# Performance work log

Measured on AMD Instinct MI355X. Metric: run time of the kernel, lower is better.

## Reference

```python
import jax, jax.numpy as jnp
import numpy as np

N_NODES = 20000
N_EDGES = 40000
NODE_DIM = 5
EDGE_DIM = 6
HIDDEN = 64
N_GRAPHS = 500
NODES_PER_GRAPH = 40
TORSIONS = 10
ACTION_DIM = 6


def _lstm_cell(x, h, c, wih, whh, bih, bhh):
    g = x @ wih.T + bih + h @ whh.T + bhh
    i, f, gg, o = jnp.split(g, 4, axis=-1)
    c = jax.nn.sigmoid(f) * c + jax.nn.sigmoid(i) * jnp.tanh(gg)
    return jax.nn.sigmoid(o) * jnp.tanh(c), c


def _gru_cell(x, h, wih, whh, bih, bhh):
    gi = x @ wih.T + bih
    gh = h @ whh.T + bhh
    ir, iz, inn = jnp.split(gi, 3, axis=-1)
    hr, hz, hn = jnp.split(gh, 3, axis=-1)
    r = jax.nn.sigmoid(ir + hr)
    z = jax.nn.sigmoid(iz + hz)
    n = jnp.tanh(inn + r * hn)
    return (1.0 - z) * n + z * h


def setup_inputs() -> dict:
    key = jax.random.key(0)
    ks = jax.random.split(key, 20)
    def gl(k, shape, fan_in):
        return jax.random.normal(k, shape, dtype=jnp.float32) / np.sqrt(float(fan_in))
    H = HIDDEN
    inp = {}
    inp['x'] = jax.random.normal(ks[0], (N_NODES, NODE_DIM), dtype=jnp.float32)
    inp['edge_attr'] = jax.random.normal(ks[1], (N_EDGES, EDGE_DIM), dtype=jnp.float32)
    inp['edge_index'] = jax.random.randint(ks[2], (2, N_EDGES), 0, N_NODES)
    inp['batch'] = jnp.arange(N_NODES) // NODES_PER_GRAPH
    g = jnp.arange(N_GRAPHS * TORSIONS) // TORSIONS
    inp['nrbidx'] = g
    local = jax.random.randint(ks[3], (N_GRAPHS * TORSIONS, 4), 0, NODES_PER_GRAPH)
    inp['nonring'] = local + (g * NODES_PER_GRAPH)[:, None]
    inp['lin0_w'] = gl(ks[4], (H, NODE_DIM), NODE_DIM); inp['lin0_b'] = jnp.zeros(H)
    inp['enn_w1'] = gl(ks[5], (128, EDGE_DIM), EDGE_DIM); inp['enn_b1'] = jnp.zeros(128)
    inp['enn_w2'] = gl(ks[6], (H * H, 128), 128) * 0.1; inp['enn_b2'] = jnp.zeros(H * H)
    inp['conv_root'] = gl(ks[7], (H, H), H); inp['conv_bias'] = jnp.zeros(H)
    inp['gru_wih'] = gl(ks[8], (3 * H, H), H); inp['gru_whh'] = gl(ks[9], (3 * H, H), H)
    inp['gru_bih'] = jnp.zeros(3 * H); inp['gru_bhh'] = jnp.zeros(3 * H)
    inp['s2s_wih'] = gl(ks[10], (4 * H, 2 * H), 2 * H); inp['s2s_whh'] = gl(ks[11], (4 * H, H), H)
    inp['s2s_bih'] = jnp.zeros(4 * H); inp['s2s_bhh'] = jnp.zeros(4 * H)
    inp['mem_wih'] = gl(ks[12], (4 * H, 2 * H), 2 * H); inp['mem_whh'] = gl(ks[13], (4 * H, H), H)
    inp['mem_bih'] = jnp.zeros(4 * H); inp['mem_bhh'] = jnp.zeros(4 * H)
    inp['mlp_w1'] = gl(ks[14], (H, 5 * H), 5 * H); inp['mlp_b1'] = jnp.zeros(H)
    inp['mlp_w2'] = gl(ks[15], (ACTION_DIM, H), H); inp['mlp_b2'] = jnp.zeros(ACTION_DIM)
    return inp


def _forward(x, edge_attr, edge_index, batch, nonring, nrbidx,
             lin0_w, lin0_b, enn_w1, enn_b1, enn_w2, enn_b2, conv_root, conv_bias,
             gru_wih, gru_whh, gru_bih, gru_bhh,
             s2s_wih, s2s_whh, s2s_bih, s2s_bhh,
             mem_wih, mem_whh, mem_bih, mem_bhh,
             mlp_w1, mlp_b1, mlp_w2, mlp_b2):
    n_nodes = x.shape[0]
    H = lin0_w.shape[0]
    N = N_GRAPHS
    src, dst = edge_index[0], edge_index[1]
    out = jax.nn.relu(x @ lin0_w.T + lin0_b)                                   # [n_nodes, H]
    ew = (jax.nn.relu(edge_attr @ enn_w1.T + enn_b1) @ enn_w2.T + enn_b2)
    ew = ew.reshape(-1, H, H)                                                  # [E, H, H] (edge-attr only -> hoisted out of loop)
    deg = jnp.maximum(jax.ops.segment_sum(jnp.ones((edge_index.shape[1],), x.dtype), dst, num_segments=n_nodes), 1.0)
    h = out
    for _ in range(6):
        msg = jnp.einsum('eh,ehk->ek', out[src], ew)                           # per-edge message
        agg = jax.ops.segment_sum(msg, dst, num_segments=n_nodes) / deg[:, None]
        m = jax.nn.relu(agg + out @ conv_root + conv_bias)
        h = _gru_cell(m, h, gru_wih, gru_whh, gru_bih, gru_bhh)
        out = h
    # --- Set2Set pooling, 6 processing steps ---
    q_star = jnp.zeros((N, 2 * H), x.dtype)
    hs = jnp.zeros((N, H), x.dtype)
    cs = jnp.zeros((N, H), x.dtype)
    for _ in range(6):
        hs, cs = _lstm_cell(q_star, hs, cs, s2s_wih, s2s_whh, s2s_bih, s2s_bhh)
        e = jnp.sum(out * hs[batch], axis=-1)                                  # [n_nodes]
        emax = jax.ops.segment_max(e, batch, num_segments=N)
        a = jnp.exp(e - emax[batch])
        a = a / jax.ops.segment_sum(a, batch, num_segments=N)[batch]
        r = jax.ops.segment_sum(a[:, None] * out, batch, num_segments=N)
        q_star = jnp.concatenate([hs, r], axis=-1)                             # [N, 2H]
    # --- memory LSTM (one step, zero initial state) ---
    hx = jnp.zeros((N, H), x.dtype)
    cx = jnp.zeros((N, H), x.dtype)
    hx, cx = _lstm_cell(q_star, hx, cx, mem_wih, mem_whh, mem_bih, mem_bhh)
    # --- gather + concat + MLP + reshape to padded [N, T, A] ---
    t_mem = hx[nrbidx]                                                         # [n_torsions, H]
    t_nodes = out[nonring.reshape(-1)].reshape(-1, 4 * H)                      # [n_torsions, 4H]
    feat = jnp.concatenate([t_mem, t_nodes], axis=-1)                          # [n_torsions, 5H]
    logits = jax.nn.relu(feat @ mlp_w1.T + mlp_b1) @ mlp_w2.T + mlp_b2
    logit = logits.reshape(N, TORSIONS, -1)                                    # uniform torsion_list_sizes -> pad_sequence is a reshape
    return logit, hx[None], cx[None]


def reference(x, edge_attr, edge_index, batch, nonring, nrbidx,
              lin0_w, lin0_b, enn_w1, enn_b1, enn_w2, enn_b2, conv_root, conv_bias,
              gru_wih, gru_whh, gru_bih, gru_bhh,
              s2s_wih, s2s_whh, s2s_bih, s2s_bhh,
              mem_wih, mem_whh, mem_bih, mem_bhh,
              mlp_w1, mlp_b1, mlp_w2, mlp_b2):
    return _forward(x, edge_attr, edge_index, batch, nonring, nrbidx,
                    lin0_w, lin0_b, enn_w1, enn_b1, enn_w2, enn_b2, conv_root, conv_bias,
                    gru_wih, gru_whh, gru_bih, gru_bhh,
                    s2s_wih, s2s_whh, s2s_bih, s2s_bhh,
                    mem_wih, mem_whh, mem_bih, mem_bhh,
                    mlp_w1, mlp_b1, mlp_w2, mlp_b2)
```

## Files before the change

kernel.cpp:

```cpp
#include <hip/hip_runtime.h>
#include <hip/hip_bf16.h>
#include <stdint.h>

#define N_NODES 20000
#define N_EDGES 40000
#define NODE_DIM 5
#define EDGE_DIM 6
#define HID 64
#define N_GRAPHS 500
#define NPG 40
#define TORSIONS 10
#define N_TORS (N_GRAPHS * TORSIONS)
#define ACT 6

typedef short short8 __attribute__((ext_vector_type(8)));
typedef float f32x4 __attribute__((ext_vector_type(4)));

__device__ __forceinline__ float sigmoidf_(float x) { return 1.0f / (1.0f + __expf(-x)); }
__device__ __forceinline__ float dot4(float4 a, float4 b) {
    return a.x * b.x + a.y * b.y + a.z * b.z + a.w * b.w;
}

__global__ void k_lin0(const float* __restrict__ x, const float* __restrict__ w,
                       const float* __restrict__ b, float* __restrict__ out) {
    int i = blockIdx.x * blockDim.x + threadIdx.x;
    int n = i >> 6, k = i & 63;
    const float* xr = x + n * NODE_DIM;
    const float* wr = w + k * NODE_DIM;
    float s = b[k];
#pragma unroll
    for (int d = 0; d < NODE_DIM; ++d) s += xr[d] * wr[d];
    out[i] = fmaxf(s, 0.0f);
}

__global__ void k_h1(const float* __restrict__ ea, const float* __restrict__ w1,
                     const float* __restrict__ b1, __hip_bfloat16* __restrict__ h1b) {
    int i = blockIdx.x * blockDim.x + threadIdx.x;
    int e = i >> 7, j = i & 127;
    const float* er = ea + e * EDGE_DIM;
    const float* wr = w1 + j * EDGE_DIM;
    float s = b1[j];
#pragma unroll
    for (int d = 0; d < EDGE_DIM; ++d) s += er[d] * wr[d];
    h1b[i] = __float2bfloat16(fmaxf(s, 0.0f));
}

__global__ void k_prep(const float* __restrict__ w2, const float* __restrict__ b2,
                       __hip_bfloat16* __restrict__ w2pb, __hip_bfloat16* __restrict__ b2pb) {
    int i = blockIdx.x * blockDim.x + threadIdx.x;
    int cp = i >> 7, j = i & 127;
    int c = ((cp & 63) << 6) | (cp >> 6);
    w2pb[i] = __float2bfloat16(w2[c * 128 + j]);
    if (j == 0) b2pb[cp] = __float2bfloat16(b2[c]);
}

__global__ void k_prep2(const float* __restrict__ cr, const float* __restrict__ wih,
                        const float* __restrict__ whh,
                        __hip_bfloat16* __restrict__ crTb, __hip_bfloat16* __restrict__ wihb,
                        __hip_bfloat16* __restrict__ whhb) {
    int i = blockIdx.x * blockDim.x + threadIdx.x;
    if (i < 12288) {
        wihb[i] = __float2bfloat16(wih[i]);
    } else if (i < 24576) {
        whhb[i - 12288] = __float2bfloat16(whh[i - 12288]);
    } else if (i < 24576 + 4096) {
        int t = i - 24576;
        int c = t >> 6, h = t & 63;
        crTb[t] = __float2bfloat16(cr[h * 64 + c]);
    }
}

__global__ void k_deg(const int* __restrict__ ei, int* __restrict__ degi) {
    int e = blockIdx.x * blockDim.x + threadIdx.x;
    if (e >= N_EDGES) return;
    atomicAdd(&degi[ei[N_EDGES + e]], 1);
}

#define SCAN_C 79
__global__ __launch_bounds__(256) void k_scan(const int* __restrict__ degi,
                                              int* __restrict__ rowptr, int* __restrict__ cursor) {
    __shared__ int part[256];
    int t = threadIdx.x;
    int base = t * SCAN_C;
    int s = 0;
    for (int i = 0; i < SCAN_C; ++i) {
        int idx = base + i;
        if (idx < N_NODES) s += degi[idx];
    }
    part[t] = s;
    __syncthreads();
    for (int off = 1; off < 256; off <<= 1) {
        int v = (t >= off) ? part[t - off] : 0;
        __syncthreads();
        part[t] += v;
        __syncthreads();
    }
    int run = part[t] - s;
    for (int i = 0; i < SCAN_C; ++i) {
        int idx = base + i;
        if (idx < N_NODES) {
            rowptr[idx] = run;
            cursor[idx] = run;
            run += degi[idx];
        }
    }
    if (t == 0) rowptr[N_NODES] = N_EDGES;
}

__global__ void k_fill(const int* __restrict__ ei, int* __restrict__ cursor,
                       int* __restrict__ csr) {
    int e = blockIdx.x * blockDim.x + threadIdx.x;
    if (e >= N_EDGES) return;
    int d = ei[N_EDGES + e];
    int pos = atomicAdd(&cursor[d], 1);
    csr[pos] = e;
}

#define EPB 5
__global__ __launch_bounds__(512) void k_edge_msg(
    const int* __restrict__ ei, const float* __restrict__ out,
    const __hip_bfloat16* __restrict__ h1b, const __hip_bfloat16* __restrict__ w2pb,
    const __hip_bfloat16* __restrict__ b2pb, float* __restrict__ msg) {
    __shared__ __align__(16) short aS[64 * 17 * 8];
    __shared__ __align__(16) float oS[64 * 68];
    __shared__ __align__(16) float mS[64 * 9];
    int bid = blockIdx.x;
    int xg = bid & 7, kb = (bid >> 3) & 7, eg = bid >> 6;
    int ebg = eg * 8 + xg;
    if (ebg >= 125) return;
    int tid = threadIdx.x, w = tid >> 6, lane = tid & 63;
    int lm = lane & 15, lk = lane >> 4;
    int kt = (kb << 3) + w;
    const short8* W8 = (const short8*)w2pb;
    short8 afr[4][4];
#pragma unroll
    for (int hi = 0; hi < 4; ++hi)
#pragma unroll
        for (int ks = 0; ks < 4; ++ks)
            afr[hi][ks] = W8[(size_t)(kt * 64 + hi * 16 + lm) * 16 + ks * 4 + lk];
    float bb[4][4];
#pragma unroll
    for (int hi = 0; hi < 4; ++hi)
#pragma unroll
        for (int j = 0; j < 4; ++j)
            bb[hi][j] = __bfloat162float(b2pb[kt * 64 + hi * 16 + lk * 4 + j]);
    const short8* aSb8 = (const short8*)aS;
    const float4* oS4 = (const float4*)oS;
    for (int t = 0; t < EPB; ++t) {
        int e0 = (ebg * EPB + t) << 6;
        {
            const uint4* g = (const uint4*)(h1b + (size_t)e0 * 128);
            uint4* s = (uint4*)aS;
#pragma unroll
            for (int p = 0; p < 2; ++p) {
                int i = tid + 512 * p;
                s[(i >> 4) * 17 + (i & 15)] = g[i];
            }
        }
        {
            const float4* og = (const float4*)out;
            float4* s = (float4*)oS;
#pragma unroll
            for (int p = 0; p < 2; ++p) {
                int i = tid + 512 * p;
                int src = ei[e0 + (i >> 4)];
                s[(i >> 4) * 17 + (i & 15)] = og[(size_t)src * 16 + (i & 15)];
            }
        }
        __syncthreads();
#pragma unroll
        for (int ee = 0; ee < 4; ++ee) {
            short8 bfr[4];
#pragma unroll
            for (int ks = 0; ks < 4; ++ks) bfr[ks] = aSb8[(ee * 16 + lm) * 17 + ks * 4 + lk];
            float4 ofr[4];
#pragma unroll
            for (int hi = 0; hi < 4; ++hi) ofr[hi] = oS4[(ee * 16 + lm) * 17 + hi * 4 + lk];
            float p = 0.0f;
#pragma unroll
            for (int hi = 0; hi < 4; ++hi) {
                f32x4 a0 = (f32x4){0.f, 0.f, 0.f, 0.f};
                f32x4 a1 = (f32x4){0.f, 0.f, 0.f, 0.f};
                a0 = __builtin_amdgcn_mfma_f32_16x16x32_bf16(afr[hi][0], bfr[0], a0, 0, 0, 0);
                a1 = __builtin_amdgcn_mfma_f32_16x16x32_bf16(afr[hi][1], bfr[1], a1, 0, 0, 0);
                a0 = __builtin_amdgcn_mfma_f32_16x16x32_bf16(afr[hi][2], bfr[2], a0, 0, 0, 0);
                a1 = __builtin_amdgcn_mfma_f32_16x16x32_bf16(afr[hi][3], bfr[3], a1, 0, 0, 0);
                p += (a0[0] + a1[0] + bb[hi][0]) * ofr[hi].x + (a0[1] + a1[1] + bb[hi][1]) * ofr[hi].y +
                     (a0[2] + a1[2] + bb[hi][2]) * ofr[hi].z + (a0[3] + a1[3] + bb[hi][3]) * ofr[hi].w;
            }
            p += __shfl_xor(p, 16);
            p += __shfl_xor(p, 32);
            if (lane < 16) mS[(ee * 16 + lane) * 9 + w] = p;
        }
        __syncthreads();
        {
            int e = tid >> 3, kl = tid & 7;
            msg[(size_t)(e0 + e) * 64 + (kb << 3) + kl] = mS[e * 9 + kl];
        }
    }
}

__global__ __launch_bounds__(64) void k_node_fused(
    float* __restrict__ out,
    const int* __restrict__ rowptr, const int* __restrict__ csr, const float* __restrict__ msg,
    const __hip_bfloat16* __restrict__ crTb, const float* __restrict__ cb,
    const __hip_bfloat16* __restrict__ wihb, const __hip_bfloat16* __restrict__ whhb,
    const float* __restrict__ bih, const float* __restrict__ bhh) {
    __shared__ __align__(16) float Xf[16 * 68];
    __shared__ __align__(16) short Xb[16 * 72];
    __shared__ __align__(16) short Mb[16 * 72];
    int n0 = blockIdx.x << 4;
    int lane = threadIdx.x;
    {
        int r = lane >> 2, q = lane & 3;
        const float4* gv = (const float4*)(out + (size_t)(n0 + r) * 64);
        float4 v[4];
#pragma unroll
        for (int i = 0; i < 4; ++i) v[i] = gv[q * 4 + i];
        float4* sv = (float4*)Xf;
#pragma unroll
        for (int i = 0; i < 4; ++i) sv[r * 17 + q * 4 + i] = v[i];
        __hip_bfloat16* xb = (__hip_bfloat16*)Xb;
        const float* vf = (const float*)v;
#pragma unroll
        for (int i = 0; i < 16; ++i) xb[r * 72 + q * 16 + i] = __float2bfloat16(vf[i]);
    }
    __syncthreads();
    int lm = lane & 15, lk = lane >> 4;
    const short8* Xb8 = (const short8*)Xb;
    short8 ax[2];
#pragma unroll
    for (int ks = 0; ks < 2; ++ks) ax[ks] = Xb8[lm * 9 + ks * 4 + lk];
    const short8* Bc = (const short8*)crTb;
    f32x4 accr[4];
#pragma unroll
    for (int ci = 0; ci < 4; ++ci) accr[ci] = (f32x4){0.f, 0.f, 0.f, 0.f};
#pragma unroll
    for (int ks = 0; ks < 2; ++ks)
#pragma unroll
        for (int ci = 0; ci < 4; ++ci) {
            short8 b = Bc[(ci * 16 + lm) * 8 + ks * 4 + lk];
            accr[ci] = __builtin_amdgcn_mfma_f32_16x16x32_bf16(ax[ks], b, accr[ci], 0, 0, 0);
        }
    float aost[4][4];
#pragma unroll
    for (int j = 0; j < 4; ++j) {
        int n = n0 + lk * 4 + j;
        int b = rowptr[n], e_ = rowptr[n + 1];
        float s0 = 0.f, s1 = 0.f, s2 = 0.f, s3 = 0.f;
        for (int i = b; i < e_; ++i) {
            const float* mrow = msg + (size_t)csr[i] * 64;
            s0 += mrow[lm];
            s1 += mrow[16 + lm];
            s2 += mrow[32 + lm];
            s3 += mrow[48 + lm];
        }
        float inv = 1.0f / fmaxf((float)(e_ - b), 1.0f);
        aost[j][0] = s0 * inv; aost[j][1] = s1 * inv; aost[j][2] = s2 * inv; aost[j][3] = s3 * inv;
    }
    __hip_bfloat16* mb = (__hip_bfloat16*)Mb;
#pragma unroll
    for (int ci = 0; ci < 4; ++ci) {
        int col = ci * 16 + lm;
        float cbv = cb[col];
#pragma unroll
        for (int j = 0; j < 4; ++j) {
            int row = lk * 4 + j;
            float m = fmaxf(aost[j][ci] + accr[ci][j] + cbv, 0.f);
            mb[row * 72 + col] = __float2bfloat16(m);
        }
    }
    __syncthreads();
    short8 am[2];
#pragma unroll
    for (int ks = 0; ks < 2; ++ks) am[ks] = ((const short8*)Mb)[lm * 9 + ks * 4 + lk];
    const short8* Bi = (const short8*)wihb;
    const short8* Bh = (const short8*)whhb;
    f32x4 gi[12], gh[12];
#pragma unroll
    for (int ci = 0; ci < 12; ++ci) {
        gi[ci] = (f32x4){0.f, 0.f, 0.f, 0.f};
        gh[ci] = (f32x4){0.f, 0.f, 0.f, 0.f};
    }
#pragma unroll
    for (int ks = 0; ks < 2; ++ks)
#pragma unroll
        for (int ci = 0; ci < 12; ++ci) {
            short8 bi = Bi[(ci * 16 + lm) * 8 + ks * 4 + lk];
            short8 bh = Bh[(ci * 16 + lm) * 8 + ks * 4 + lk];
            gi[ci] = __builtin_amdgcn_mfma_f32_16x16x32_bf16(am[ks], bi, gi[ci], 0, 0, 0);
            gh[ci] = __builtin_amdgcn_mfma_f32_16x16x32_bf16(ax[ks], bh, gh[ci], 0, 0, 0);
        }
#pragma unroll
    for (int ci = 0; ci < 4; ++ci) {
        int col = ci * 16 + lm;
        float bir = bih[col], biz = bih[64 + col], bin = bih[128 + col];
        float bhr = bhh[col], bhz = bhh[64 + col], bhn = bhh[128 + col];
#pragma unroll
        for (int j = 0; j < 4; ++j) {
            int row = lk * 4 + j;
            int n = n0 + row;
            float r = sigmoidf_(gi[ci][j] + bir + gh[ci][j] + bhr);
            float z = sigmoidf_(gi[ci + 4][j] + biz + gh[ci + 4][j] + bhz);
            float nn = tanhf(gi[ci + 8][j] + bin + r * (gh[ci + 8][j] + bhn));
            float hold = Xf[row * 68 + col];
            out[(size_t)n * 64 + col] = (1.f - z) * nn + z * hold;
        }
    }
}

__global__ __launch_bounds__(64) void k_s2s(const float* __restrict__ out,
                                            const float* __restrict__ wih, const float* __restrict__ whh,
                                            const float* __restrict__ bih, const float* __restrict__ bhh,
                                            const float* __restrict__ mwih, const float* __restrict__ mbih,
                                            const float* __restrict__ mbhh,
                                            float* __restrict__ dout, float* __restrict__ hx_buf) {
    int g = blockIdx.x;
    int lane = threadIdx.x;
    __shared__ __align__(16) float os[NPG][65];
    __shared__ __align__(16) float q[128];
    __shared__ __align__(16) float hsS[64];
    __shared__ __align__(16) float aS[NPG];
    for (int n = 0; n < NPG; ++n) os[n][lane] = out[(size_t)(g * NPG + n) * 64 + lane];
    q[lane] = 0.0f;
    q[64 + lane] = 0.0f;
    hsS[lane] = 0.0f;
    float cs = 0.0f;
    __syncthreads();
    const float4* qv = (const float4*)q;
    const float4* hv = (const float4*)hsS;
    for (int step = 0; step < 6; ++step) {
        float gate[4];
#pragma unroll
        for (int gg = 0; gg < 4; ++gg) {
            int j = gg * 64 + lane;
            const float4* wr = (const float4*)(wih + (size_t)j * 128);
            const float4* vr = (const float4*)(whh + (size_t)j * 64);
            float s = bih[j] + bhh[j];
#pragma unroll 8
            for (int i = 0; i < 32; ++i) s += dot4(qv[i], wr[i]);
#pragma unroll 8
            for (int i = 0; i < 16; ++i) s += dot4(hv[i], vr[i]);
            gate[gg] = s;
        }
        cs = sigmoidf_(gate[1]) * cs + sigmoidf_(gate[0]) * tanhf(gate[2]);
        float hsv = sigmoidf_(gate[3]) * tanhf(cs);
        __syncthreads();
        hsS[lane] = hsv;
        __syncthreads();
        float e_n = -INFINITY;
        if (lane < NPG) {
            float s = 0.0f;
            for (int h = 0; h < 64; ++h) s += os[lane][h] * hsS[h];
            e_n = s;
        }
        float mx = e_n;
#pragma unroll
        for (int off = 32; off; off >>= 1) mx = fmaxf(mx, __shfl_xor(mx, off));
        float ex = (lane < NPG) ? __expf(e_n - mx) : 0.0f;
        float sm = ex;
#pragma unroll
        for (int off = 32; off; off >>= 1) sm += __shfl_xor(sm, off);
        if (lane < NPG) aS[lane] = ex / sm;
        __syncthreads();
        float r = 0.0f;
        for (int n = 0; n < NPG; ++n) r += aS[n] * os[n][lane];
        __syncthreads();
        q[lane] = hsv;
        q[64 + lane] = r;
        __syncthreads();
    }
    float gate[4];
#pragma unroll
    for (int gg = 0; gg < 4; ++gg) {
        int j = gg * 64 + lane;
        const float4* wr = (const float4*)(mwih + (size_t)j * 128);
        float s = mbih[j] + mbhh[j];
#pragma unroll 8
        for (int i = 0; i < 32; ++i) s += dot4(qv[i], wr[i]);
        gate[gg] = s;
    }
    float cx = sigmoidf_(gate[0]) * tanhf(gate[2]);
    float hx = sigmoidf_(gate[3]) * tanhf(cx);
    dout[30000 + g * 64 + lane] = hx;
    dout[62000 + g * 64 + lane] = cx;
    hx_buf[g * 64 + lane] = hx;
}

__global__ __launch_bounds__(256) void k_mlp(const float* __restrict__ out,
                                             const float* __restrict__ hx_buf,
                                             const int* __restrict__ nrbidx,
                                             const int* __restrict__ nonring,
                                             const float* __restrict__ w1, const float* __restrict__ b1,
                                             const float* __restrict__ w2, const float* __restrict__ b2,
                                             float* __restrict__ logits) {
    __shared__ __align__(16) float feat[4][320];
    __shared__ __align__(16) float hid[4][64];
    int w = threadIdx.x >> 6, lane = threadIdx.x & 63;
    int t = (blockIdx.x << 2) + w;
    int g = nrbidx[t];
    feat[w][lane] = hx_buf[g * 64 + lane];
#pragma unroll
    for (int i = 0; i < 4; ++i) {
        int node = nonring[t * 4 + i];
        feat[w][64 + i * 64 + lane] = out[(size_t)node * 64 + lane];
    }
    __syncthreads();
    const float4* fv = (const float4*)feat[w];
    const float4* wr = (const float4*)(w1 + (size_t)lane * 320);
    float s = b1[lane];
#pragma unroll 8
    for (int i = 0; i < 80; ++i) s += dot4(fv[i], wr[i]);
    hid[w][lane] = fmaxf(s, 0.0f);
    __syncthreads();
    if (lane < ACT) {
        const float* hr = hid[w];
        const float* w2r = w2 + lane * 64;
        float s2 = b2[lane];
#pragma unroll 8
        for (int k = 0; k < 64; ++k) s2 += hr[k] * w2r[k];
        logits[t * ACT + lane] = s2;
    }
}

static inline size_t align256(size_t x) { return (x + 255) & ~(size_t)255; }

extern "C" void kernel_launch(void* const* d_in, const int* in_sizes, int n_in,
                              void* d_out, int out_size, void* d_ws, size_t ws_size,
                              hipStream_t stream) {
    const float* x         = (const float*)d_in[0];
    const float* edge_attr = (const float*)d_in[1];
    const int*   edge_index= (const int*)d_in[2];
    const int*   nrbidx    = (const int*)d_in[4];
    const int*   nonring   = (const int*)d_in[5];
    const float* lin0_w    = (const float*)d_in[6];
    const float* lin0_b    = (const float*)d_in[7];
    const float* enn_w1    = (const float*)d_in[8];
    const float* enn_b1    = (const float*)d_in[9];
    const float* enn_w2    = (const float*)d_in[10];
    const float* enn_b2    = (const float*)d_in[11];
    const float* conv_root = (const float*)d_in[12];
    const float* conv_bias = (const float*)d_in[13];
    const float* gru_wih   = (const float*)d_in[14];
    const float* gru_whh   = (const float*)d_in[15];
    const float* gru_bih   = (const float*)d_in[16];
    const float* gru_bhh   = (const float*)d_in[17];
    const float* s2s_wih   = (const float*)d_in[18];
    const float* s2s_whh   = (const float*)d_in[19];
    const float* s2s_bih   = (const float*)d_in[20];
    const float* s2s_bhh   = (const float*)d_in[21];
    const float* mem_wih   = (const float*)d_in[22];
    const float* mem_bih   = (const float*)d_in[24];
    const float* mem_bhh   = (const float*)d_in[25];
    const float* mlp_w1    = (const float*)d_in[26];
    const float* mlp_b1    = (const float*)d_in[27];
    const float* mlp_w2    = (const float*)d_in[28];
    const float* mlp_b2    = (const float*)d_in[29];
    float* dout = (float*)d_out;

    char* ws = (char*)d_ws;
    size_t off = 0;
    float* out_buf = (float*)(ws + off); off = align256(off + (size_t)N_NODES * 64 * 4);
    float* msg     = (float*)(ws + off); off = align256(off + (size_t)N_EDGES * 64 * 4);
    __hip_bfloat16* h1b  = (__hip_bfloat16*)(ws + off); off = align256(off + (size_t)N_EDGES * 128 * 2);
    __hip_bfloat16* w2pb = (__hip_bfloat16*)(ws + off); off = align256(off + (size_t)4096 * 128 * 2);
    __hip_bfloat16* b2pb = (__hip_bfloat16*)(ws + off); off = align256(off + 4096 * 2);
    int* degi      = (int*)(ws + off); off = align256(off + N_NODES * 4);
    int* rowptr    = (int*)(ws + off); off = align256(off + (N_NODES + 1) * 4);
    int* cursor    = (int*)(ws + off); off = align256(off + N_NODES * 4);
    int* csr       = (int*)(ws + off); off = align256(off + N_EDGES * 4);
    float* hx_buf  = (float*)(ws + off); off = align256(off + (size_t)N_GRAPHS * 64 * 4);
    __hip_bfloat16* wihb = (__hip_bfloat16*)(ws + off); off = align256(off + 192 * 64 * 2);
    __hip_bfloat16* whhb = (__hip_bfloat16*)(ws + off); off = align256(off + 192 * 64 * 2);
    __hip_bfloat16* crTb = (__hip_bfloat16*)(ws + off); off = align256(off + 64 * 64 * 2);
    if (ws_size < off) return;

    k_lin0<<<(N_NODES * 64) / 256, 256, 0, stream>>>(x, lin0_w, lin0_b, out_buf);
    k_h1<<<(N_EDGES * 128) / 256, 256, 0, stream>>>(edge_attr, enn_w1, enn_b1, h1b);
    k_prep<<<(4096 * 128) / 256, 256, 0, stream>>>(enn_w2, enn_b2, w2pb, b2pb);
    k_prep2<<<112, 256, 0, stream>>>(conv_root, gru_wih, gru_whh, crTb, wihb, whhb);
    hipMemsetAsync(degi, 0, N_NODES * 4, stream);
    k_deg<<<(N_EDGES + 255) / 256, 256, 0, stream>>>(edge_index, degi);
    k_scan<<<1, 256, 0, stream>>>(degi, rowptr, cursor);
    k_fill<<<(N_EDGES + 255) / 256, 256, 0, stream>>>(edge_index, cursor, csr);
    for (int it = 0; it < 6; ++it) {
        k_edge_msg<<<1024, 512, 0, stream>>>(edge_index, out_buf, h1b, w2pb, b2pb, msg);
        k_node_fused<<<N_NODES / 16, 64, 0, stream>>>(out_buf, rowptr, csr, msg, crTb, conv_bias,
                                                      wihb, whhb, gru_bih, gru_bhh);
    }
    k_s2s<<<N_GRAPHS, 64, 0, stream>>>(out_buf, s2s_wih, s2s_whh, s2s_bih, s2s_bhh,
                                       mem_wih, mem_bih, mem_bhh, dout, hx_buf);
    k_mlp<<<N_TORS / 4, 256, 0, stream>>>(out_buf, hx_buf, nrbidx, nonring,
                                          mlp_w1, mlp_b1, mlp_w2, mlp_b2, dout);
}
```

Measured before the change: 776.0 us.

## Widen Set2Set kernel to 256 threads and stage edge bias in LDS

The Set2Set LSTM kernel moves from one wavefront per graph to four. Each thread now computes one of the 256 gate rows, the LSTM update runs in the first wave, and the attention readout is split across waves with a partial-sum reduction. This shortens the serial per-graph critical path, at the cost of more barriers and shared-memory traffic. Separately, in the edge-message kernel the per-thread bias registers are replaced by a small LDS-staged bf16 bias that is read and unpacked inline, which is meant to lower register pressure.

```diff
diff --git a/kernel.cpp b/kernel.cpp
--- a/kernel.cpp
+++ b/kernel.cpp
@@ -19,6 +19,12 @@
 __device__ __forceinline__ float sigmoidf_(float x) { return 1.0f / (1.0f + __expf(-x)); }
 __device__ __forceinline__ float dot4(float4 a, float4 b) {
     return a.x * b.x + a.y * b.y + a.z * b.z + a.w * b.w;
+}
+__device__ __forceinline__ float bf_lo(unsigned int u) {
+    union { unsigned int i; float f; } v; v.i = u << 16; return v.f;
+}
+__device__ __forceinline__ float bf_hi(unsigned int u) {
+    union { unsigned int i; float f; } v; v.i = u & 0xffff0000u; return v.f;
 }
 
 __global__ void k_lin0(const float* __restrict__ x, const float* __restrict__ w,
@@ -124,6 +130,7 @@
     __shared__ __align__(16) short aS[64 * 17 * 8];
     __shared__ __align__(16) float oS[64 * 68];
     __shared__ __align__(16) float mS[64 * 9];
+    __shared__ __align__(8)  short bS[512];
     int bid = blockIdx.x;
     int xg = bid & 7, kb = (bid >> 3) & 7, eg = bid >> 6;
     int ebg = eg * 8 + xg;
@@ -138,12 +145,7 @@
 #pragma unroll
         for (int ks = 0; ks < 4; ++ks)
             afr[hi][ks] = W8[(size_t)(kt * 64 + hi * 16 + lm) * 16 + ks * 4 + lk];
-    float bb[4][4];
-#pragma unroll
-    for (int hi = 0; hi < 4; ++hi)
-#pragma unroll
-        for (int j = 0; j < 4; ++j)
-            bb[hi][j] = __bfloat162float(b2pb[kt * 64 + hi * 16 + lk * 4 + j]);
+    bS[tid] = ((const short*)b2pb)[(kb << 9) + tid];
     const short8* aSb8 = (const short8*)aS;
     const float4* oS4 = (const float4*)oS;
     for (int t = 0; t < EPB; ++t) {
@@ -185,8 +187,11 @@
                 a1 = __builtin_amdgcn_mfma_f32_16x16x32_bf16(afr[hi][1], bfr[1], a1, 0, 0, 0);
                 a0 = __builtin_amdgcn_mfma_f32_16x16x32_bf16(afr[hi][2], bfr[2], a0, 0, 0, 0);
                 a1 = __builtin_amdgcn_mfma_f32_16x16x32_bf16(afr[hi][3], bfr[3], a1, 0, 0, 0);
-                p += (a0[0] + a1[0] + bb[hi][0]) * ofr[hi].x + (a0[1] + a1[1] + bb[hi][1]) * ofr[hi].y +
-                     (a0[2] + a1[2] + bb[hi][2]) * ofr[hi].z + (a0[3] + a1[3] + bb[hi][3]) * ofr[hi].w;
+                uint2 bp = *(const uint2*)(bS + (w << 6) + hi * 16 + lk * 4);
+                p += (a0[0] + a1[0] + bf_lo(bp.x)) * ofr[hi].x +
+                     (a0[1] + a1[1] + bf_hi(bp.x)) * ofr[hi].y +
+                     (a0[2] + a1[2] + bf_lo(bp.y)) * ofr[hi].z +
+                     (a0[3] + a1[3] + bf_hi(bp.y)) * ofr[hi].w;
             }
             p += __shfl_xor(p, 16);
             p += __shfl_xor(p, 32);
@@ -309,82 +314,91 @@
     }
 }
 
-__global__ __launch_bounds__(64) void k_s2s(const float* __restrict__ out,
-                                            const float* __restrict__ wih, const float* __restrict__ whh,
-                                            const float* __restrict__ bih, const float* __restrict__ bhh,
-                                            const float* __restrict__ mwih, const float* __restrict__ mbih,
-                                            const float* __restrict__ mbhh,
-                                            float* __restrict__ dout, float* __restrict__ hx_buf) {
+__global__ __launch_bounds__(256) void k_s2s(const float* __restrict__ out,
+                                             const float* __restrict__ wih, const float* __restrict__ whh,
+                                             const float* __restrict__ bih, const float* __restrict__ bhh,
+                                             const float* __restrict__ mwih, const float* __restrict__ mbih,
+                                             const float* __restrict__ mbhh,
+                                             float* __restrict__ dout, float* __restrict__ hx_buf) {
     int g = blockIdx.x;
-    int lane = threadIdx.x;
+    int tid = threadIdx.x;
+    int w = tid >> 6, lane = tid & 63;
     __shared__ __align__(16) float os[NPG][65];
     __shared__ __align__(16) float q[128];
     __shared__ __align__(16) float hsS[64];
+    __shared__ __align__(16) float csS[64];
     __shared__ __align__(16) float aS[NPG];
-    for (int n = 0; n < NPG; ++n) os[n][lane] = out[(size_t)(g * NPG + n) * 64 + lane];
-    q[lane] = 0.0f;
-    q[64 + lane] = 0.0f;
-    hsS[lane] = 0.0f;
-    float cs = 0.0f;
+    __shared__ __align__(16) float gS[256];
+    __shared__ __align__(16) float rP[4][64];
+    for (int idx = tid; idx < NPG * 64; idx += 256)
+        os[idx >> 6][idx & 63] = out[(size_t)(g * NPG) * 64 + idx];
+    if (tid < 128) q[tid] = 0.0f;
+    if (tid < 64) { hsS[tid] = 0.0f; csS[tid] = 0.0f; }
     __syncthreads();
     const float4* qv = (const float4*)q;
     const float4* hv = (const float4*)hsS;
     for (int step = 0; step < 6; ++step) {
-        float gate[4];
-#pragma unroll
-        for (int gg = 0; gg < 4; ++gg) {
-            int j = gg * 64 + lane;
-            const float4* wr = (const float4*)(wih + (size_t)j * 128);
-            const float4* vr = (const float4*)(whh + (size_t)j * 64);
-            float s = bih[j] + bhh[j];
+        {
+            const float4* wr = (const float4*)(wih + (size_t)tid * 128);
+            const float4* vr = (const float4*)(whh + (size_t)tid * 64);
+            float s = bih[tid] + bhh[tid];
 #pragma unroll 8
             for (int i = 0; i < 32; ++i) s += dot4(qv[i], wr[i]);
 #pragma unroll 8
             for (int i = 0; i < 16; ++i) s += dot4(hv[i], vr[i]);
-            gate[gg] = s;
-        }
-        cs = sigmoidf_(gate[1]) * cs + sigmoidf_(gate[0]) * tanhf(gate[2]);
-        float hsv = sigmoidf_(gate[3]) * tanhf(cs);
-        __syncthreads();
-        hsS[lane] = hsv;
-        __syncthreads();
-        float e_n = -INFINITY;
-        if (lane < NPG) {
-            float s = 0.0f;
-            for (int h = 0; h < 64; ++h) s += os[lane][h] * hsS[h];
-            e_n = s;
-        }
-        float mx = e_n;
-#pragma unroll
-        for (int off = 32; off; off >>= 1) mx = fmaxf(mx, __shfl_xor(mx, off));
-        float ex = (lane < NPG) ? __expf(e_n - mx) : 0.0f;
-        float sm = ex;
-#pragma unroll
-        for (int off = 32; off; off >>= 1) sm += __shfl_xor(sm, off);
-        if (lane < NPG) aS[lane] = ex / sm;
-        __syncthreads();
-        float r = 0.0f;
-        for (int n = 0; n < NPG; ++n) r += aS[n] * os[n][lane];
-        __syncthreads();
-        q[lane] = hsv;
-        q[64 + lane] = r;
-        __syncthreads();
-    }
-    float gate[4];
-#pragma unroll
-    for (int gg = 0; gg < 4; ++gg) {
-        int j = gg * 64 + lane;
-        const float4* wr = (const float4*)(mwih + (size_t)j * 128);
-        float s = mbih[j] + mbhh[j];
+            gS[tid] = s;
+        }
+        __syncthreads();
+        if (tid < 64) {
+            float cs = sigmoidf_(gS[64 + tid]) * csS[tid] + sigmoidf_(gS[tid]) * tanhf(gS[128 + tid]);
+            csS[tid] = cs;
+            hsS[tid] = sigmoidf_(gS[192 + tid]) * tanhf(cs);
+        }
+        __syncthreads();
+        if (w == 0) {
+            float e_n = -INFINITY;
+            if (lane < NPG) {
+                float s = 0.0f;
+                for (int h = 0; h < 64; ++h) s += os[lane][h] * hsS[h];
+                e_n = s;
+            }
+            float mx = e_n;
+#pragma unroll
+            for (int off = 32; off; off >>= 1) mx = fmaxf(mx, __shfl_xor(mx, off));
+            float ex = (lane < NPG) ? __expf(e_n - mx) : 0.0f;
+            float sm = ex;
+#pragma unroll
+            for (int off = 32; off; off >>= 1) sm += __shfl_xor(sm, off);
+            if (lane < NPG) aS[lane] = ex / sm;
+        }
+        __syncthreads();
+        {
+            float r = 0.0f;
+            for (int n = w * 10; n < w * 10 + 10; ++n) r += aS[n] * os[n][lane];
+            rP[w][lane] = r;
+        }
+        __syncthreads();
+        if (tid < 64) {
+            q[tid] = hsS[tid];
+            q[64 + tid] = rP[0][tid] + rP[1][tid] + rP[2][tid] + rP[3][tid];
+        }
+        __syncthreads();
+    }
+    {
+        const float4* wr = (const float4*)(mwih + (size_t)tid * 128);
+        float s = mbih[tid] + mbhh[tid];
 #pragma unroll 8
         for (int i = 0; i < 32; ++i) s += dot4(qv[i], wr[i]);
-        gate[gg] = s;
-    }
-    float cx = sigmoidf_(gate[0]) * tanhf(gate[2]);
-    float hx = sigmoidf_(gate[3]) * tanhf(cx);
-    dout[30000 + g * 64 + lane] = hx;
-    dout[62000 + g * 64 + lane] = cx;
-    hx_buf[g * 64 + lane] = hx;
+        gS[tid] = s;
+    }
+    __syncthreads();
+    if (tid < 64) {
+        float cx = sigmoidf_(gS[tid]) * tanhf(gS[128 + tid]);
+        float hx = sigmoidf_(gS[192 + tid]) * tanhf(cx);
+        dout[30000 + g * 64 + tid] = hx;
+        dout[62000 + g * 64 + tid] = cx;
+        hx_buf[g * 64 + tid] = hx;
+    }
 }
 
 __global__ __launch_bounds__(256) void k_mlp(const float* __restrict__ out,
@@ -488,8 +502,8 @@
         k_node_fused<<<N_NODES / 16, 64, 0, stream>>>(out_buf, rowptr, csr, msg, crTb, conv_bias,
                                                       wihb, whhb, gru_bih, gru_bhh);
     }
-    k_s2s<<<N_GRAPHS, 64, 0, stream>>>(out_buf, s2s_wih, s2s_whh, s2s_bih, s2s_bhh,
-                                       mem_wih, mem_bih, mem_bhh, dout, hx_buf);
+    k_s2s<<<N_GRAPHS, 256, 0, stream>>>(out_buf, s2s_wih, s2s_whh, s2s_bih, s2s_bhh,
+                                        mem_wih, mem_bih, mem_bhh, dout, hx_buf);
     k_mlp<<<N_TORS / 4, 256, 0, stream>>>(out_buf, hx_buf, nrbidx, nonring,
                                           mlp_w1, mlp_b1, mlp_w2, mlp_b2, dout);
 }
```

Result: slower. 803.0 us (+3.5%).
